# Optimization experiments

Hardware: AMD Instinct MI355X
Metric: run time of the kernel (lower is better)

## Reference

```python
import jax, jax.numpy as jnp
import numpy as np

N = 65536      # tokens
C = 192        # input_size
O = 192        # output_size
H = 384        # hidden_size
E = 8          # num_experts
B = 4          # num_bands
R = 8          # lora_rank
ALPHA = 16.0   # lora_alpha
F = 64         # dct_freq_features
CF = 1.25      # capacity_factor
M = 2          # max_fanout_per_token
LN_EPS = 1e-5
LOSS_COEF = 0.01
K = min(max(1, int(N / float(E) * CF)), N)  # expert capacity = 10240


def setup_inputs() -> dict:
    key = jax.random.key(0)
    ks = jax.random.split(key, 18)
    s = 0.02
    gin = C + F + 2
    x = jax.random.normal(ks[0], (N, C), jnp.float32)
    x_prev = x + 0.1 * jax.random.normal(ks[1], (N, C), jnp.float32)
    bw = jax.random.uniform(ks[2], (N, B), jnp.float32)
    bw = bw / bw.sum(axis=1, keepdims=True)
    return {
        'x': x,
        'band_weights': bw,
        'x_prev_tokens': x_prev,
        'Wz': s * jax.random.normal(ks[3], (C, F), jnp.float32),        # linear extractor (no bias)
        'ln_g': jnp.ones((gin,), jnp.float32),
        'ln_b': jnp.zeros((gin,), jnp.float32),
        'Wg': s * jax.random.normal(ks[4], (gin, E), jnp.float32),
        'bg': s * jax.random.normal(ks[5], (E,), jnp.float32),
        'W1': s * jax.random.normal(ks[6], (E, C, H), jnp.float32),
        'b1': s * jax.random.normal(ks[7], (E, H), jnp.float32),
        'W2': s * jax.random.normal(ks[8], (E, H, O), jnp.float32),
        'b2': s * jax.random.normal(ks[9], (E, O), jnp.float32),
        'A1': s * jax.random.normal(ks[10], (E, B, C, R), jnp.float32),
        'B1': s * jax.random.normal(ks[11], (E, B, R, H), jnp.float32),
        'A2': s * jax.random.normal(ks[12], (E, B, H, R), jnp.float32),
        'B2': s * jax.random.normal(ks[13], (E, B, R, O), jnp.float32),
    }


def _cv_squared(v):
    m = v.mean()
    var = ((v - m) ** 2).mean()  # population var (correction=0)
    return var / (m * m + 1e-10)


def reference(x, band_weights, x_prev_tokens, Wz, ln_g, ln_b, Wg, bg,
              W1, b1, W2, b2, A1, B1, A2, B2):
    # --- DAFE features (inference path: EMA buffer == detached extractor out) ---
    Z = jax.lax.stop_gradient(x @ Wz)                        # [N, F]
    # --- residual hint (detached) ---
    delta = jax.lax.stop_gradient(x - x_prev_tokens)
    a = jnp.abs(delta)
    mu = jnp.log1p(a.mean(axis=1, keepdims=True))
    sd = jnp.log1p(a.std(axis=1, keepdims=True, ddof=1))     # torch std: unbiased
    et = jnp.concatenate([x, Z, mu, sd], axis=1)             # [N, C+F+2]
    # --- gate LayerNorm ---
    m_ = et.mean(axis=-1, keepdims=True)
    v_ = ((et - m_) ** 2).mean(axis=-1, keepdims=True)
    et = (et - m_) * jax.lax.rsqrt(v_ + LN_EPS) * ln_g + ln_b
    # --- gating logits (fp32, temperature == 1.0) ---
    logits = et.astype(jnp.float32) @ Wg + bg                # [N, E]
    # --- expert-choice: each expert picks top-K tokens ---
    _, ti = jax.lax.top_k(logits.T, K)                       # [E, K]
    mask = jnp.zeros((N, E), bool).at[ti, jnp.arange(E)[:, None]].set(True)
    # cover tokens picked by no expert with their argmax expert
    unc = ~mask.any(axis=1)
    best = jnp.argmax(logits, axis=1)
    mask = mask | (unc[:, None] & (jnp.arange(E)[None, :] == best[:, None]))
    # --- per-token sparse softmax over top-M candidate experts ---
    masked = jnp.where(mask, logits, -jnp.inf)
    sel_logits, topm = jax.lax.top_k(masked, M)              # [N, M]
    sel_w = jax.nn.softmax(sel_logits, axis=-1)              # -inf rows -> weight 0
    gw = jnp.zeros((N, E), x.dtype).at[jnp.arange(N)[:, None], topm].set(sel_w.astype(x.dtype))
    # --- experts: shared MLP + band-weighted LoRA on both layers ---
    scale = ALPHA / R
    out = jnp.zeros((N, O), x.dtype)
    for e in range(E):  # small fixed expert count
        t1 = jnp.einsum('nc,bcr->nbr', x, A1[e])
        u1 = jnp.einsum('nbr,brh,nb->nh', t1, B1[e], band_weights)
        h = jax.nn.gelu(x @ W1[e] + b1[e] + scale * u1, approximate=False)
        t2 = jnp.einsum('nh,bhr->nbr', h, A2[e])
        u2 = jnp.einsum('nbr,bro,nb->no', t2, B2[e], band_weights)
        ye = h @ W2[e] + b2[e] + scale * u2
        out = out + gw[:, e:e + 1] * ye                      # zero gate == not dispatched
    # --- load-balance aux loss ---
    importance = gw.sum(axis=0)
    load = (gw > 0).sum(axis=0).astype(jnp.float32)
    loss = (_cv_squared(importance) + _cv_squared(load)) * LOSS_COEF
    return out, loss
```

## Files before the change

kernel.cpp:

```cpp
#include <hip/hip_runtime.h>
#include <hip/hip_bf16.h>
#include <math.h>

constexpr int N = 65536;
constexpr int C = 192;
constexpr int O = 192;
constexpr int H = 384;
constexpr int E = 8;
constexpr int B = 4;
constexpr int R = 8;
constexpr int F = 64;
constexpr int GIN = C + F + 2;
constexpr int K = 10240;
constexpr int TM = 32;
constexpr int NBKT = 16384;
constexpr int PCH = 16;
constexpr int CAP = 32768;
constexpr int GT = 32;

typedef unsigned short ushort;
typedef __attribute__((ext_vector_type(8))) short bf16x8;
typedef __attribute__((ext_vector_type(4))) float f32x4;
typedef __attribute__((ext_vector_type(4))) double f64x4;
typedef __attribute__((ext_vector_type(4))) ushort ushort4v;

#define MFMA(a, b, c) __builtin_amdgcn_mfma_f32_16x16x32_bf16(a, b, c, 0, 0, 0)
#define DMFMA(a, b, c) __builtin_amdgcn_mfma_f64_16x16x4f64(a, b, c, 0, 0, 0)

__device__ inline ushort f2bf(float f) {
  union { float f; unsigned u; } v; v.f = f;
  unsigned r = v.u + 0x7FFFu + ((v.u >> 16) & 1u);
  return (ushort)(r >> 16);
}

__device__ inline unsigned long long dkey(double d) {
  unsigned long long u = (unsigned long long)__double_as_longlong(d);
  return (u & 0x8000000000000000ULL) ? ~u : (u | 0x8000000000000000ULL);
}

__device__ inline double wave_reduce_sum(double v) {
  #pragma unroll
  for (int off = 32; off; off >>= 1) v += __shfl_down(v, off);
  return v;
}

__global__ __launch_bounds__(256) void convert_kernel(
    const float* __restrict__ W1, const float* __restrict__ W2,
    const float* __restrict__ A1, const float* __restrict__ B1,
    const float* __restrict__ A2, const float* __restrict__ B2,
    const float* __restrict__ ln_g, const float* __restrict__ ln_b,
    const float* __restrict__ Wg,
    ushort* __restrict__ W1t, ushort* __restrict__ W2t,
    ushort* __restrict__ A1t, ushort* __restrict__ B1t,
    ushort* __restrict__ A2t, ushort* __restrict__ B2t,
    double* __restrict__ C0g, double* __restrict__ CBg) {
  const int s1 = E * H * C;
  const int s2 = E * O * H;
  const int s3 = E * 32 * C;
  const int s4 = E * H * 32;
  const int s5 = E * 32 * H;
  const int s6 = E * O * 32;
  if (blockIdx.x == 0 && threadIdx.x < 16) {
    int e = threadIdx.x & 7;
    double acc = 0.0;
    if (threadIdx.x < 8) {
      for (int i = 0; i < GIN; ++i) acc += (double)ln_g[i] * (double)Wg[i * E + e];
      C0g[e] = acc;
    } else {
      for (int i = 0; i < GIN; ++i) acc += (double)ln_b[i] * (double)Wg[i * E + e];
      CBg[e] = acc;
    }
  }
  int tid = blockIdx.x * 256 + threadIdx.x;
  if (tid < s1) {
    int e = tid / (H * C), rem = tid % (H * C), h = rem / C, c = rem % C;
    W1t[tid] = f2bf(W1[((size_t)e * C + c) * H + h]);
  } else if ((tid -= s1) < s2) {
    int e = tid / (O * H), rem = tid % (O * H), o = rem / H, h = rem % H;
    W2t[tid] = f2bf(W2[((size_t)e * H + h) * O + o]);
  } else if ((tid -= s2) < s3) {
    int e = tid / (32 * C), rem = tid % (32 * C), br = rem / C, c = rem % C;
    int b = br >> 3, r = br & 7;
    A1t[tid] = f2bf(A1[(((size_t)e * B + b) * C + c) * R + r]);
  } else if ((tid -= s3) < s4) {
    int e = tid / (H * 32), rem = tid % (H * 32), h = rem / 32, br = rem % 32;
    B1t[tid] = f2bf(B1[((size_t)e * 32 + br) * H + h]);
  } else if ((tid -= s4) < s5) {
    int e = tid / (32 * H), rem = tid % (32 * H), br = rem / H, h = rem % H;
    int b = br >> 3, r = br & 7;
    A2t[tid] = f2bf(A2[(((size_t)e * B + b) * H + h) * R + r]);
  } else if ((tid -= s5) < s6) {
    int e = tid / (O * 32), rem = tid % (O * 32), o = rem / 32, br = rem % 32;
    B2t[tid] = f2bf(B2[((size_t)e * 32 + br) * O + o]);
  }
}

__global__ __launch_bounds__(512, 4) void gate_kernel(
    const float* __restrict__ x, const float* __restrict__ xp,
    const float* __restrict__ Wz, const float* __restrict__ ln_g,
    const float* __restrict__ ln_b, const float* __restrict__ Wg,
    const float* __restrict__ bg, const double* __restrict__ C0g,
    const double* __restrict__ CBg, double* __restrict__ logitsT) {
  __shared__ float xs[GT][196];
  __shared__ double Zs[GT][65];
  __shared__ double Wgp[256][10];
  __shared__ double Sp[2][16][10];
  __shared__ double Sfin[GT][12];
  __shared__ double Sfz[GT][12];
  __shared__ double s2zs[GT];
  __shared__ double mus[GT], sds[GT], sxs[GT], s2xs[GT];

  int tid = threadIdx.x;
  int n0 = blockIdx.x * GT;
  int w = tid >> 6, lane = tid & 63;
  int arow = lane & 15, kg = lane >> 4;
  int tt = w >> 2, ft = w & 3;

  for (int u = tid; u < 256 * 8; u += 512) {
    int k = u >> 3, e = u & 7;
    Wgp[k][e] = (double)ln_g[k] * (double)Wg[k * E + e];
  }
  if (tid < 256) { Wgp[tid][8] = 1.0; Wgp[tid][9] = 0.0; }

  {
    int t = tid >> 4, ch = tid & 15;
    const float* xr = x + (size_t)(n0 + t) * C + ch * 12;
    const float* pr = xp + (size_t)(n0 + t) * C + ch * 12;
    double pa = 0.0, pa2 = 0.0, px = 0.0, px2 = 0.0;
    #pragma unroll
    for (int j = 0; j < 3; ++j) {
      float4 xv = *(const float4*)(xr + j * 4);
      float4 pv = *(const float4*)(pr + j * 4);
      *(float4*)&xs[t][ch * 12 + j * 4] = xv;
      float xa[4] = {xv.x, xv.y, xv.z, xv.w};
      float pp[4] = {pv.x, pv.y, pv.z, pv.w};
      #pragma unroll
      for (int q2 = 0; q2 < 4; ++q2) {
        double dx = (double)xa[q2];
        px += dx; px2 += dx * dx;
        double ad = (double)fabsf(xa[q2] - pp[q2]);
        pa += ad; pa2 += ad * ad;
      }
    }
    #pragma unroll
    for (int off = 8; off; off >>= 1) {
      pa += __shfl_down(pa, off);
      pa2 += __shfl_down(pa2, off);
      px += __shfl_down(px, off);
      px2 += __shfl_down(px2, off);
    }
    if (ch == 0) {
      double mean_a = pa * (1.0 / 192.0);
      double var_a = (pa2 - pa * pa * (1.0 / 192.0)) * (1.0 / 191.0);
      var_a = var_a > 0.0 ? var_a : 0.0;
      mus[t] = log1p(mean_a);
      sds[t] = log1p(sqrt(var_a));
      sxs[t] = px; s2xs[t] = px2;
    }
  }

  int rowIdx[4], colIdx[4];
  {
    f64x4 z4 = {0.0, 0.0, 0.0, 0.0};
    double pr = (double)arow;
    double pk = (kg == 0) ? 1.0 : 0.0;
    f64x4 p1 = DMFMA(pr, pk, z4);
    f64x4 p2 = DMFMA(pk, pr, z4);
    #pragma unroll
    for (int d = 0; d < 4; ++d) {
      rowIdx[d] = ((int)p1[d]) & 15;
      colIdx[d] = ((int)p2[d]) & 15;
    }
  }

  __syncthreads();

  {
    f64x4 acc[2];
    acc[0] = (f64x4){0.0, 0.0, 0.0, 0.0}; acc[1] = acc[0];
    float bxa[24];
    #pragma unroll
    for (int s = 0; s < 24; ++s)
      bxa[s] = Wz[(4 * s + kg) * F + ft * 16 + arow];
    #pragma unroll
    for (int s = 0; s < 24; ++s) {
      double a = (double)xs[tt * 16 + arow][4 * s + kg];
      acc[s & 1] = DMFMA(a, (double)bxa[s], acc[s & 1]);
    }
    #pragma unroll
    for (int s = 0; s < 24; ++s)
      bxa[s] = Wz[(96 + 4 * s + kg) * F + ft * 16 + arow];
    #pragma unroll
    for (int s = 0; s < 24; ++s) {
      double a = (double)xs[tt * 16 + arow][96 + 4 * s + kg];
      acc[s & 1] = DMFMA(a, (double)bxa[s], acc[s & 1]);
    }
    f64x4 r = acc[0] + acc[1];
    #pragma unroll
    for (int d = 0; d < 4; ++d)
      Zs[tt * 16 + rowIdx[d]][ft * 16 + colIdx[d]] = r[d];
  }
  __syncthreads();

  int ccol = arow < 9 ? arow : 9;
  f64x4 rx = {0.0, 0.0, 0.0, 0.0};
  int xt2 = 0;
  if (w < 4) {
    int t2 = w >> 1, kh = w & 1; xt2 = t2;
    int kbase = kh * 96;
    f64x4 acc[2];
    acc[0] = (f64x4){0.0, 0.0, 0.0, 0.0}; acc[1] = acc[0];
    #pragma unroll
    for (int s = 0; s < 24; ++s) {
      int k = kbase + 4 * s + kg;
      double a = (double)xs[t2 * 16 + arow][k];
      acc[s & 1] = DMFMA(a, Wgp[k][ccol], acc[s & 1]);
    }
    f64x4 r = acc[0] + acc[1];
    if (kh == 0) {
      #pragma unroll
      for (int d = 0; d < 4; ++d)
        if (colIdx[d] < 9) Sp[t2][rowIdx[d]][colIdx[d]] = r[d];
    } else {
      rx = r;
    }
  } else {
    int zq = w - 4; int t2 = zq & 1; int sq = zq >> 1;
    f64x4 acc[2];
    acc[0] = (f64x4){0.0, 0.0, 0.0, 0.0}; acc[1] = acc[0];
    #pragma unroll
    for (int s = 0; s < 16; ++s) {
      double a = Zs[t2 * 16 + arow][4 * s + kg];
      if (sq) a = a * a;
      acc[s & 1] = DMFMA(a, Wgp[192 + 4 * s + kg][ccol], acc[s & 1]);
    }
    f64x4 r = acc[0] + acc[1];
    if (!sq) {
      #pragma unroll
      for (int d = 0; d < 4; ++d)
        if (colIdx[d] < 9) Sfz[t2 * 16 + rowIdx[d]][colIdx[d]] = r[d];
    } else {
      #pragma unroll
      for (int d = 0; d < 4; ++d)
        if (colIdx[d] == 8) s2zs[t2 * 16 + rowIdx[d]] = r[d];
    }
  }
  __syncthreads();
  if (w < 4 && (w & 1)) {
    #pragma unroll
    for (int d = 0; d < 4; ++d)
      if (colIdx[d] < 9)
        Sfin[xt2 * 16 + rowIdx[d]][colIdx[d]] =
            rx[d] + Sp[xt2][rowIdx[d]][colIdx[d]];
  }
  __syncthreads();

  if (tid < GT * E) {
    int t = tid >> 3, e = tid & 7;
    int n = n0 + t;
    double mu = mus[t], sd = sds[t];
    double s = sxs[t] + Sfz[t][8] + mu + sd;
    double q = s2xs[t] + s2zs[t] + mu * mu + sd * sd;
    double m_ = s * (1.0 / 258.0);
    double v_ = q * (1.0 / 258.0) - m_ * m_;
    v_ = v_ > 0.0 ? v_ : 0.0;
    double rstd = 1.0 / sqrt(v_ + 1e-5);
    double G256e = (double)ln_g[256] * (double)Wg[256 * E + e];
    double G257e = (double)ln_g[257] * (double)Wg[257 * E + e];
    double S = Sfin[t][e] + Sfz[t][e] + mu * G256e + sd * G257e;
    double logit = rstd * S - rstd * m_ * C0g[e] + CBg[e] + (double)bg[e];
    logitsT[(size_t)e * N + n] = logit;
  }
}

__global__ __launch_bounds__(256) void selA_kernel(
    const double* __restrict__ logitsT, unsigned* __restrict__ gh) {
  __shared__ unsigned hist[NBKT];
  int e = blockIdx.y;
  const double* L = logitsT + (size_t)e * N + blockIdx.x * (N / PCH);
  for (int i = threadIdx.x; i < NBKT; i += 256) hist[i] = 0;
  __syncthreads();
  for (int i = threadIdx.x; i < N / PCH; i += 256) {
    unsigned long long k = dkey(L[i]);
    atomicAdd(&hist[(unsigned)(k >> 50)], 1u);
  }
  __syncthreads();
  unsigned* ghe = gh + (size_t)e * NBKT;
  for (int i = threadIdx.x; i < NBKT; i += 256) {
    unsigned v = hist[i];
    if (v) atomicAdd(&ghe[i], v);
  }
}

__global__ __launch_bounds__(256) void selB_kernel(
    const unsigned* __restrict__ gh, int* __restrict__ boundB,
    int* __restrict__ countAbove) {
  int e = blockIdx.x;
  const unsigned* ghe = gh + (size_t)e * NBKT;
  __shared__ unsigned chunkSum[256];
  unsigned s = 0;
  int base = threadIdx.x * 64;
  for (int i = 0; i < 64; ++i) s += ghe[base + i];
  chunkSum[threadIdx.x] = s;
  __syncthreads();
  if (threadIdx.x == 0) {
    long long acc = 0;
    for (int t = 255; t >= 0; --t) {
      if (acc + (long long)chunkSum[t] >= K) {
        for (int b = t * 64 + 63; b >= t * 64; --b) {
          unsigned hv = ghe[b];
          if (acc + (long long)hv >= K) {
            boundB[e] = b; countAbove[e] = (int)acc; return;
          }
          acc += hv;
        }
      }
      acc += chunkSum[t];
    }
    boundB[e] = 0; countAbove[e] = 0;
  }
}

__global__ __launch_bounds__(256) void selC_kernel(
    const double* __restrict__ logitsT, const int* __restrict__ boundB,
    int* __restrict__ candCnt, unsigned long long* __restrict__ candKey,
    int* __restrict__ candIdx) {
  int e = blockIdx.y;
  unsigned bb = (unsigned)boundB[e];
  int base = blockIdx.x * (N / PCH);
  const double* L = logitsT + (size_t)e * N;
  int lane = threadIdx.x & 63;
  unsigned long long below = (1ULL << lane) - 1ULL;
  for (int i0 = 0; i0 < N / PCH; i0 += 256) {
    int n = base + i0 + threadIdx.x;
    unsigned long long k = dkey(L[n]);
    bool match = ((unsigned)(k >> 50) == bb);
    unsigned long long mk = __ballot(match);
    if (match) {
      int leader = __ffsll((long long)mk) - 1;
      int cbase = 0;
      if (lane == leader) cbase = atomicAdd(&candCnt[e], __popcll(mk));
      cbase = __shfl(cbase, leader);
      int pos = cbase + __popcll(mk & below);
      if (pos < CAP) {
        candKey[(size_t)e * CAP + pos] = k;
        candIdx[(size_t)e * CAP + pos] = n;
      }
    }
  }
}

__global__ __launch_bounds__(256) void selD_kernel(
    const unsigned long long* __restrict__ candKey, const int* __restrict__ candIdx,
    const int* __restrict__ candCnt, const int* __restrict__ countAbove,
    unsigned long long* __restrict__ Tkey, int* __restrict__ tieCut) {
  int e = blockIdx.x;
  int c = candCnt[e]; if (c > CAP) c = CAP;
  int need = K - countAbove[e];
  const unsigned long long* keys = candKey + (size_t)e * CAP;
  const int* idxs = candIdx + (size_t)e * CAP;
  __shared__ unsigned hist[256];
  __shared__ unsigned long long spref;
  __shared__ int srem;
  __shared__ int red[256];
  int tid = threadIdx.x;
  if (tid == 0) { spref = 0ULL; srem = need; }
  __syncthreads();
  for (int pass = 7; pass >= 0; --pass) {
    hist[tid] = 0;
    __syncthreads();
    unsigned long long pref = spref;
    unsigned long long mhi = (pass == 7) ? 0ULL : (~0ULL << ((pass + 1) * 8));
    for (int i = tid; i < c; i += 256) {
      unsigned long long k = keys[i];
      if ((k & mhi) == pref)
        atomicAdd(&hist[(unsigned)((k >> (pass * 8)) & 0xFF)], 1u);
    }
    __syncthreads();
    if (tid == 0) {
      int rem = srem;
      int b = 255;
      for (; b > 0; --b) {
        int cc = (int)hist[b];
        if (cc >= rem) break;
        rem -= cc;
      }
      srem = rem;
      spref = pref | ((unsigned long long)(unsigned)b << (pass * 8));
    }
    __syncthreads();
  }
  unsigned long long T = spref;
  int needT = srem;
  int lo = 0, hi = N - 1;
  while (lo < hi) {
    int mid = (lo + hi) >> 1;
    int cnt = 0;
    for (int i = tid; i < c; i += 256)
      cnt += (keys[i] == T && idxs[i] <= mid) ? 1 : 0;
    red[tid] = cnt;
    __syncthreads();
    for (int off = 128; off; off >>= 1) {
      if (tid < off) red[tid] += red[tid + off];
      __syncthreads();
    }
    int total = red[0];
    __syncthreads();
    if (total >= needT) hi = mid; else lo = mid + 1;
  }
  if (tid == 0) { Tkey[e] = T; tieCut[e] = lo; }
}

__global__ __launch_bounds__(256) void route_kernel(
    const double* __restrict__ logitsT, const unsigned long long* __restrict__ Tkey,
    const int* __restrict__ tieCut, int* __restrict__ cnt,
    int* __restrict__ list_tok, float* __restrict__ list_w,
    double* __restrict__ importance) {
  int n = blockIdx.x * 256 + threadIdx.x;
  int lane = threadIdx.x & 63;
  double l[E];
  unsigned selbits = 0;
  #pragma unroll
  for (int e = 0; e < E; ++e) {
    l[e] = logitsT[(size_t)e * N + n];
    unsigned long long k = dkey(l[e]);
    unsigned long long T = Tkey[e];
    bool sel = (k > T) || (k == T && n <= tieCut[e]);
    if (sel) selbits |= (1u << e);
  }
  if (selbits == 0) {
    int best = 0; double bv = l[0];
    #pragma unroll
    for (int e = 1; e < E; ++e) if (l[e] > bv) { bv = l[e]; best = e; }
    selbits = (1u << best);
  }
  int i0 = -1, i1 = -1;
  double v0 = -1e300, v1 = -1e300;
  #pragma unroll
  for (int e = 0; e < E; ++e) {
    if (selbits & (1u << e)) {
      double v = l[e];
      if (v > v0) { v1 = v0; i1 = i0; v0 = v; i0 = e; }
      else if (v > v1) { v1 = v; i1 = e; }
    }
  }
  double w0 = 1.0, w1 = 0.0;
  if (i1 >= 0) {
    double e1 = exp(v1 - v0);
    w0 = 1.0 / (1.0 + e1);
    w1 = e1 / (1.0 + e1);
  }
  float w0f = (float)w0;
  float w1f = (float)w1;
  bool app1 = (i1 >= 0) && (w1f > 0.0f);

  unsigned long long below = (1ULL << lane) - 1ULL;
  #pragma unroll
  for (int e = 0; e < E; ++e) {
    unsigned long long m0 = __ballot(i0 == e);
    unsigned long long m1 = __ballot(app1 && i1 == e);
    int c = __popcll(m0) + __popcll(m1);
    int basep = 0;
    if (lane == 0 && c) basep = atomicAdd(&cnt[e], c);
    basep = __shfl(basep, 0);
    if (i0 == e) {
      int idx = basep + __popcll(m0 & below);
      list_tok[e * N + idx] = n;
      list_w[e * N + idx] = w0f;
    }
    if (app1 && i1 == e) {
      int idx = basep + __popcll(m0) + __popcll(m1 & below);
      list_tok[e * N + idx] = n;
      list_w[e * N + idx] = w1f;
    }
    double v = 0.0;
    if (i0 == e) v += (double)w0f;
    if (app1 && i1 == e) v += (double)w1f;
    v = wave_reduce_sum(v);
    if (lane == 0 && v != 0.0) unsafeAtomicAdd(&importance[e], v);
  }
}

__global__ __launch_bounds__(256) void expert_kernel(
    const float* __restrict__ x, const float* __restrict__ bw,
    const float* __restrict__ b1g, const float* __restrict__ b2g,
    const ushort* __restrict__ W1t, const ushort* __restrict__ W2t,
    const ushort* __restrict__ A1t, const ushort* __restrict__ B1t,
    const ushort* __restrict__ A2t, const ushort* __restrict__ B2t,
    const int* __restrict__ cnt, const int* __restrict__ list_tok,
    const float* __restrict__ list_w, float* __restrict__ out) {
  int e = blockIdx.y;
  int ce = cnt[e];
  int start = blockIdx.x * TM;
  if (start >= ce) return;
  int m = ce - start; if (m > TM) m = TM;

  __shared__ ushort xs[TM][200];
  __shared__ ushort hs[TM][392];
  __shared__ ushort t1w[TM][40];
  __shared__ ushort t2w[TM][40];
  __shared__ int stok[TM];
  __shared__ float swt[TM];
  __shared__ float bws[TM][B];

  int tid = threadIdx.x;
  if (tid < TM) {
    int idx = start + (tid < m ? tid : 0);
    stok[tid] = list_tok[e * N + idx];
    swt[tid] = (tid < m) ? list_w[e * N + idx] : 0.0f;
  }
  __syncthreads();
  for (int u = tid; u < TM * 48; u += 256) {
    int t = u / 48, ch = u % 48;
    float4 v = *(const float4*)(x + (size_t)stok[t] * C + ch * 4);
    ushort4v o4;
    o4.x = f2bf(v.x); o4.y = f2bf(v.y); o4.z = f2bf(v.z); o4.w = f2bf(v.w);
    *(ushort4v*)&xs[t][ch * 4] = o4;
  }
  if (tid < TM * B) {
    int t = tid >> 2, b = tid & 3;
    bws[t][b] = bw[(size_t)stok[t] * B + b];
  }
  __syncthreads();

  int w = tid >> 6, lane = tid & 63, q = lane >> 4, mr = lane & 15;

  {
    int mt = w >> 1, nt = w & 1;
    const ushort* A1te = A1t + ((size_t)e * 32 + nt * 16 + mr) * C;
    f32x4 acc = {0.f, 0.f, 0.f, 0.f};
    #pragma unroll
    for (int ks = 0; ks < 6; ++ks) {
      bf16x8 a = *(const bf16x8*)&xs[mt * 16 + mr][ks * 32 + q * 8];
      bf16x8 b = *(const bf16x8*)(A1te + ks * 32 + q * 8);
      acc = MFMA(a, b, acc);
    }
    int brc = nt * 16 + mr, bb = brc >> 3;
    #pragma unroll
    for (int r = 0; r < 4; ++r) {
      int t = mt * 16 + q * 4 + r;
      t1w[t][brc] = f2bf(2.0f * acc[r] * bws[t][bb]);
    }
  }
  __syncthreads();

  {
    const ushort* W1te = W1t + (size_t)e * H * C;
    const ushort* B1te = B1t + (size_t)e * H * 32;
    for (int ht = w * 6; ht < w * 6 + 6; ++ht) {
      int h = ht * 16 + mr;
      float bi = b1g[e * H + h];
      f32x4 acc0 = {bi, bi, bi, bi}, acc1 = acc0;
      bf16x8 bb = *(const bf16x8*)(B1te + h * 32 + q * 8);
      acc0 = MFMA(*(const bf16x8*)&t1w[mr][q * 8], bb, acc0);
      acc1 = MFMA(*(const bf16x8*)&t1w[16 + mr][q * 8], bb, acc1);
      #pragma unroll
      for (int ks = 0; ks < 6; ++ks) {
        bf16x8 wb = *(const bf16x8*)(W1te + (size_t)h * C + ks * 32 + q * 8);
        acc0 = MFMA(*(const bf16x8*)&xs[mr][ks * 32 + q * 8], wb, acc0);
        acc1 = MFMA(*(const bf16x8*)&xs[16 + mr][ks * 32 + q * 8], wb, acc1);
      }
      #pragma unroll
      for (int r = 0; r < 4; ++r) {
        float v0 = acc0[r], v1 = acc1[r];
        v0 = 0.5f * v0 * (1.0f + erff(v0 * 0.70710678118654752f));
        v1 = 0.5f * v1 * (1.0f + erff(v1 * 0.70710678118654752f));
        hs[q * 4 + r][h] = f2bf(v0);
        hs[16 + q * 4 + r][h] = f2bf(v1);
      }
    }
  }
  __syncthreads();

  {
    int mt = w >> 1, nt = w & 1;
    const ushort* A2te = A2t + ((size_t)e * 32 + nt * 16 + mr) * H;
    f32x4 acc = {0.f, 0.f, 0.f, 0.f};
    #pragma unroll
    for (int ks = 0; ks < 12; ++ks) {
      bf16x8 a = *(const bf16x8*)&hs[mt * 16 + mr][ks * 32 + q * 8];
      bf16x8 b = *(const bf16x8*)(A2te + ks * 32 + q * 8);
      acc = MFMA(a, b, acc);
    }
    int brc = nt * 16 + mr, bb = brc >> 3;
    #pragma unroll
    for (int r = 0; r < 4; ++r) {
      int t = mt * 16 + q * 4 + r;
      t2w[t][brc] = f2bf(2.0f * acc[r] * bws[t][bb]);
    }
  }
  __syncthreads();

  {
    const ushort* W2te = W2t + (size_t)e * O * H;
    const ushort* B2te = B2t + (size_t)e * O * 32;
    for (int ot = w * 3; ot < w * 3 + 3; ++ot) {
      int o = ot * 16 + mr;
      float bi = b2g[e * O + o];
      f32x4 acc0 = {bi, bi, bi, bi}, acc1 = acc0;
      bf16x8 bb = *(const bf16x8*)(B2te + o * 32 + q * 8);
      acc0 = MFMA(*(const bf16x8*)&t2w[mr][q * 8], bb, acc0);
      acc1 = MFMA(*(const bf16x8*)&t2w[16 + mr][q * 8], bb, acc1);
      #pragma unroll
      for (int ks = 0; ks < 12; ++ks) {
        bf16x8 wb = *(const bf16x8*)(W2te + (size_t)o * H + ks * 32 + q * 8);
        acc0 = MFMA(*(const bf16x8*)&hs[mr][ks * 32 + q * 8], wb, acc0);
        acc1 = MFMA(*(const bf16x8*)&hs[16 + mr][ks * 32 + q * 8], wb, acc1);
      }
      #pragma unroll
      for (int r = 0; r < 4; ++r) {
        int t0 = q * 4 + r, t1i = 16 + q * 4 + r;
        if (t0 < m)
          unsafeAtomicAdd(&out[(size_t)stok[t0] * O + o], swt[t0] * acc0[r]);
        if (t1i < m)
          unsafeAtomicAdd(&out[(size_t)stok[t1i] * O + o], swt[t1i] * acc1[r]);
      }
    }
  }
}

__global__ void loss_kernel(const double* __restrict__ importance,
                            const int* __restrict__ cnt,
                            float* __restrict__ loss_out) {
  if (threadIdx.x == 0 && blockIdx.x == 0) {
    double im = 0.0, lm = 0.0;
    for (int e = 0; e < E; ++e) { im += importance[e]; lm += (double)cnt[e]; }
    im *= (1.0 / E); lm *= (1.0 / E);
    double iv = 0.0, lv = 0.0;
    for (int e = 0; e < E; ++e) {
      double di = importance[e] - im; iv += di * di;
      double dl = (double)cnt[e] - lm; lv += dl * dl;
    }
    iv *= (1.0 / E); lv *= (1.0 / E);
    double loss = (iv / (im * im + 1e-10) + lv / (lm * lm + 1e-10)) * 0.01;
    loss_out[0] = (float)loss;
  }
}

extern "C" void kernel_launch(void* const* d_in, const int* in_sizes, int n_in,
                              void* d_out, int out_size, void* d_ws, size_t ws_size,
                              hipStream_t stream) {
  const float* x    = (const float*)d_in[0];
  const float* bw   = (const float*)d_in[1];
  const float* xp   = (const float*)d_in[2];
  const float* Wz   = (const float*)d_in[3];
  const float* ln_g = (const float*)d_in[4];
  const float* ln_b = (const float*)d_in[5];
  const float* Wg   = (const float*)d_in[6];
  const float* bg   = (const float*)d_in[7];
  const float* W1   = (const float*)d_in[8];
  const float* b1   = (const float*)d_in[9];
  const float* W2   = (const float*)d_in[10];
  const float* b2   = (const float*)d_in[11];
  const float* A1   = (const float*)d_in[12];
  const float* B1   = (const float*)d_in[13];
  const float* A2   = (const float*)d_in[14];
  const float* B2   = (const float*)d_in[15];
  float* out = (float*)d_out;

  const size_t MB = 1024 * 1024;
  char* ws = (char*)d_ws;
  double* logitsT = (double*)ws;
  int*    list_tok = (int*)(ws + 4 * MB);
  float*  list_w   = (float*)(ws + 6 * MB);
  char*   hdr      = ws + 8 * MB;
  unsigned long long* Tkey = (unsigned long long*)hdr;
  int*    tieCut = (int*)(hdr + 64);
  int*    cnt    = (int*)(hdr + 96);
  double* importance = (double*)(hdr + 128);
  int*    boundB = (int*)(hdr + 256);
  int*    countAbove = (int*)(hdr + 288);
  int*    candCnt = (int*)(hdr + 320);
  double* C0g = (double*)(hdr + 512);
  double* CBg = (double*)(hdr + 576);
  ushort* W1t = (ushort*)(ws + 8 * MB + 4096);
  ushort* W2t = W1t + (size_t)E * H * C;
  ushort* A1t = W2t + (size_t)E * O * H;
  ushort* B1t = A1t + (size_t)E * 32 * C;
  ushort* A2t = B1t + (size_t)E * H * 32;
  ushort* B2t = A2t + (size_t)E * 32 * H;
  unsigned* gh = (unsigned*)(ws + 12 * MB);
  unsigned long long* candKey = (unsigned long long*)(ws + 13 * MB);
  int* candIdx = (int*)(ws + 15 * MB);

  hipMemsetAsync(d_out, 0, (size_t)(N * O + 1) * sizeof(float), stream);
  hipMemsetAsync(hdr + 96, 0, 352 - 96, stream);
  hipMemsetAsync(gh, 0, (size_t)E * NBKT * sizeof(unsigned), stream);

  int convN = (E * H * C) * 2 + (E * 32 * C) * 2 + (E * H * 32) * 2;
  convert_kernel<<<(convN + 255) / 256, 256, 0, stream>>>(
      W1, W2, A1, B1, A2, B2, ln_g, ln_b, Wg,
      W1t, W2t, A1t, B1t, A2t, B2t, C0g, CBg);
  gate_kernel<<<N / GT, 512, 0, stream>>>(x, xp, Wz, ln_g, ln_b, Wg, bg,
                                          C0g, CBg, logitsT);
  selA_kernel<<<dim3(PCH, E), 256, 0, stream>>>(logitsT, gh);
  selB_kernel<<<E, 256, 0, stream>>>(gh, boundB, countAbove);
  selC_kernel<<<dim3(PCH, E), 256, 0, stream>>>(logitsT, boundB, candCnt,
                                                candKey, candIdx);
  selD_kernel<<<E, 256, 0, stream>>>(candKey, candIdx, candCnt, countAbove,
                                     Tkey, tieCut);
  route_kernel<<<N / 256, 256, 0, stream>>>(logitsT, Tkey, tieCut, cnt,
                                            list_tok, list_w, importance);
  expert_kernel<<<dim3(N / TM, E), 256, 0, stream>>>(
      x, bw, b1, b2, W1t, W2t, A1t, B1t, A2t, B2t, cnt, list_tok, list_w, out);
  loss_kernel<<<1, 64, 0, stream>>>(importance, cnt, out + (size_t)N * O);
}
```

Before: 724.2 us.

## Double expert token tile to 64 with 512-thread blocks for weight reuse

The expert kernel now processes 64 routed tokens per block with 8 waves instead of 32 tokens with 4. Each wave's W1 tile loop runs four MFMA accumulator chains, so each global weight fragment serves twice as many tokens. The W2 stage splits its output tiles across waves by row half. LDS is trimmed by merging the two LoRA staging buffers, storing token ids as ushort, and storing band weights in bf16 with the 2x scale folded in. The cost is a much larger LDS footprint per block, which may limit blocks per CU, and lower precision on the band weights.

Result: slower. 778.0 us (+7.4%).

```diff
diff --git a/kernel.cpp b/kernel.cpp
--- a/kernel.cpp
+++ b/kernel.cpp
@@ -12,7 +12,7 @@
 constexpr int F = 64;
 constexpr int GIN = C + F + 2;
 constexpr int K = 10240;
-constexpr int TM = 32;
+constexpr int TM = 64;
 constexpr int NBKT = 16384;
 constexpr int PCH = 16;
 constexpr int CAP = 32768;
@@ -31,6 +31,11 @@
   union { float f; unsigned u; } v; v.f = f;
   unsigned r = v.u + 0x7FFFu + ((v.u >> 16) & 1u);
   return (ushort)(r >> 16);
+}
+
+__device__ inline float bf2f(ushort u) {
+  union { unsigned u; float f; } v; v.u = ((unsigned)u) << 16;
+  return v.f;
 }
 
 __device__ inline unsigned long long dkey(double d) {
@@ -481,7 +486,7 @@
   }
 }
 
-__global__ __launch_bounds__(256) void expert_kernel(
+__global__ __launch_bounds__(512, 4) void expert_kernel(
     const float* __restrict__ x, const float* __restrict__ bw,
     const float* __restrict__ b1g, const float* __restrict__ b2g,
     const ushort* __restrict__ W1t, const ushort* __restrict__ W2t,
@@ -497,20 +502,19 @@
 
   __shared__ ushort xs[TM][200];
   __shared__ ushort hs[TM][392];
-  __shared__ ushort t1w[TM][40];
-  __shared__ ushort t2w[TM][40];
-  __shared__ int stok[TM];
+  __shared__ ushort tw[TM][40];
+  __shared__ ushort stok[TM];
   __shared__ float swt[TM];
-  __shared__ float bws[TM][B];
+  __shared__ ushort bws[TM][B];
 
   int tid = threadIdx.x;
   if (tid < TM) {
     int idx = start + (tid < m ? tid : 0);
-    stok[tid] = list_tok[e * N + idx];
+    stok[tid] = (ushort)list_tok[e * N + idx];
     swt[tid] = (tid < m) ? list_w[e * N + idx] : 0.0f;
   }
   __syncthreads();
-  for (int u = tid; u < TM * 48; u += 256) {
+  for (int u = tid; u < TM * 48; u += 512) {
     int t = u / 48, ch = u % 48;
     float4 v = *(const float4*)(x + (size_t)stok[t] * C + ch * 4);
     ushort4v o4;
@@ -519,7 +523,7 @@
   }
   if (tid < TM * B) {
     int t = tid >> 2, b = tid & 3;
-    bws[t][b] = bw[(size_t)stok[t] * B + b];
+    bws[t][b] = f2bf(2.0f * bw[(size_t)stok[t] * B + b]);
   }
   __syncthreads();
 
@@ -539,7 +543,7 @@
     #pragma unroll
     for (int r = 0; r < 4; ++r) {
       int t = mt * 16 + q * 4 + r;
-      t1w[t][brc] = f2bf(2.0f * acc[r] * bws[t][bb]);
+      tw[t][brc] = f2bf(acc[r] * bf2f(bws[t][bb]));
     }
   }
   __syncthreads();
@@ -547,26 +551,34 @@
   {
     const ushort* W1te = W1t + (size_t)e * H * C;
     const ushort* B1te = B1t + (size_t)e * H * 32;
-    for (int ht = w * 6; ht < w * 6 + 6; ++ht) {
+    for (int ht = w * 3; ht < w * 3 + 3; ++ht) {
       int h = ht * 16 + mr;
       float bi = b1g[e * H + h];
-      f32x4 acc0 = {bi, bi, bi, bi}, acc1 = acc0;
+      f32x4 acc0 = {bi, bi, bi, bi}, acc1 = acc0, acc2 = acc0, acc3 = acc0;
       bf16x8 bb = *(const bf16x8*)(B1te + h * 32 + q * 8);
-      acc0 = MFMA(*(const bf16x8*)&t1w[mr][q * 8], bb, acc0);
-      acc1 = MFMA(*(const bf16x8*)&t1w[16 + mr][q * 8], bb, acc1);
+      acc0 = MFMA(*(const bf16x8*)&tw[mr][q * 8], bb, acc0);
+      acc1 = MFMA(*(const bf16x8*)&tw[16 + mr][q * 8], bb, acc1);
+      acc2 = MFMA(*(const bf16x8*)&tw[32 + mr][q * 8], bb, acc2);
+      acc3 = MFMA(*(const bf16x8*)&tw[48 + mr][q * 8], bb, acc3);
       #pragma unroll
       for (int ks = 0; ks < 6; ++ks) {
         bf16x8 wb = *(const bf16x8*)(W1te + (size_t)h * C + ks * 32 + q * 8);
         acc0 = MFMA(*(const bf16x8*)&xs[mr][ks * 32 + q * 8], wb, acc0);
         acc1 = MFMA(*(const bf16x8*)&xs[16 + mr][ks * 32 + q * 8], wb, acc1);
+        acc2 = MFMA(*(const bf16x8*)&xs[32 + mr][ks * 32 + q * 8], wb, acc2);
+        acc3 = MFMA(*(const bf16x8*)&xs[48 + mr][ks * 32 + q * 8], wb, acc3);
       }
       #pragma unroll
       for (int r = 0; r < 4; ++r) {
-        float v0 = acc0[r], v1 = acc1[r];
+        float v0 = acc0[r], v1 = acc1[r], v2 = acc2[r], v3 = acc3[r];
         v0 = 0.5f * v0 * (1.0f + erff(v0 * 0.70710678118654752f));
         v1 = 0.5f * v1 * (1.0f + erff(v1 * 0.70710678118654752f));
+        v2 = 0.5f * v2 * (1.0f + erff(v2 * 0.70710678118654752f));
+        v3 = 0.5f * v3 * (1.0f + erff(v3 * 0.70710678118654752f));
         hs[q * 4 + r][h] = f2bf(v0);
         hs[16 + q * 4 + r][h] = f2bf(v1);
+        hs[32 + q * 4 + r][h] = f2bf(v2);
+        hs[48 + q * 4 + r][h] = f2bf(v3);
       }
     }
   }
@@ -586,7 +598,7 @@
     #pragma unroll
     for (int r = 0; r < 4; ++r) {
       int t = mt * 16 + q * 4 + r;
-      t2w[t][brc] = f2bf(2.0f * acc[r] * bws[t][bb]);
+      tw[t][brc] = f2bf(acc[r] * bf2f(bws[t][bb]));
     }
   }
   __syncthreads();
@@ -594,22 +606,26 @@
   {
     const ushort* W2te = W2t + (size_t)e * O * H;
     const ushort* B2te = B2t + (size_t)e * O * 32;
-    for (int ot = w * 3; ot < w * 3 + 3; ++ot) {
+    #pragma unroll
+    for (int i = 0; i < 3; ++i) {
+      int uo = w * 3 + i;
+      int ot = uo >> 1, sh = uo & 1;
       int o = ot * 16 + mr;
+      int r0 = sh * 32, r1 = sh * 32 + 16;
       float bi = b2g[e * O + o];
       f32x4 acc0 = {bi, bi, bi, bi}, acc1 = acc0;
       bf16x8 bb = *(const bf16x8*)(B2te + o * 32 + q * 8);
-      acc0 = MFMA(*(const bf16x8*)&t2w[mr][q * 8], bb, acc0);
-      acc1 = MFMA(*(const bf16x8*)&t2w[16 + mr][q * 8], bb, acc1);
+      acc0 = MFMA(*(const bf16x8*)&tw[r0 + mr][q * 8], bb, acc0);
+      acc1 = MFMA(*(const bf16x8*)&tw[r1 + mr][q * 8], bb, acc1);
       #pragma unroll
       for (int ks = 0; ks < 12; ++ks) {
         bf16x8 wb = *(const bf16x8*)(W2te + (size_t)o * H + ks * 32 + q * 8);
-        acc0 = MFMA(*(const bf16x8*)&hs[mr][ks * 32 + q * 8], wb, acc0);
-        acc1 = MFMA(*(const bf16x8*)&hs[16 + mr][ks * 32 + q * 8], wb, acc1);
+        acc0 = MFMA(*(const bf16x8*)&hs[r0 + mr][ks * 32 + q * 8], wb, acc0);
+        acc1 = MFMA(*(const bf16x8*)&hs[r1 + mr][ks * 32 + q * 8], wb, acc1);
       }
       #pragma unroll
       for (int r = 0; r < 4; ++r) {
-        int t0 = q * 4 + r, t1i = 16 + q * 4 + r;
+        int t0 = r0 + q * 4 + r, t1i = r1 + q * 4 + r;
         if (t0 < m)
           unsafeAtomicAdd(&out[(size_t)stok[t0] * O + o], swt[t0] * acc0[r]);
         if (t1i < m)
@@ -701,7 +717,7 @@
                                      Tkey, tieCut);
   route_kernel<<<N / 256, 256, 0, stream>>>(logitsT, Tkey, tieCut, cnt,
                                             list_tok, list_w, importance);
-  expert_kernel<<<dim3(N / TM, E), 256, 0, stream>>>(
+  expert_kernel<<<dim3(N / TM, E), 512, 0, stream>>>(
       x, bw, b1, b2, W1t, W2t, A1t, B1t, A2t, B2t, cnt, list_tok, list_w, out);
   loss_kernel<<<1, 64, 0, stream>>>(importance, cnt, out + (size_t)N * O);
 }
```
